# Kernel optimization log

Hardware: AMD Instinct MI355X
Metric: run time of the kernel (lower is better)

## Reference

```python
import jax, jax.numpy as jnp
import numpy as np

B, T = 64, 2048
HID, FAST, SLOW, VOCAB = 256, 64, 256, 64
WRITE_THRESH = 0.4
NEG = -1000000000.0


def setup_inputs() -> dict:
    key = jax.random.key(0)
    ks = jax.random.split(key, 10)
    s = 0.05  # small init so gate sigmoids are not saturated
    return {
        "seq": jax.random.randint(ks[0], (B, T), 0, VOCAB),
        "emb": jax.random.normal(ks[1], (VOCAB, HID), jnp.float32),        # encoder embedding table
        "Wg": jax.random.normal(ks[2], (HID, 1), jnp.float32) * s,         # write_gate
        "bg": jnp.zeros((1,), jnp.float32),
        "Wd": jax.random.normal(ks[3], (HID, 1), jnp.float32) * s,         # demotion_net
        "bd": jnp.zeros((1,), jnp.float32),
        "Wq": jax.random.normal(ks[4], (HID, HID), jnp.float32) * s,       # read_head.q_proj
        "bq": jnp.zeros((HID,), jnp.float32),
        "Wo": jax.random.normal(ks[5], (HID, VOCAB), jnp.float32) * s,     # read_head.out
        "bo": jnp.zeros((VOCAB,), jnp.float32),
    }


def _process_sequence(h, Wg, bg, Wd, bd):
    # h: (B, T, H). Sequential LRU tiered-memory scatter, vectorized over batch.
    Bb, Tt, H = h.shape

    def step(state, tok_h):
        fm, sm, fa, sa, fu, su = state
        ws = jax.nn.sigmoid(tok_h @ Wg + bg)[:, 0]          # (B,) write score
        act = ws >= WRITE_THRESH                            # skip rows with score < 0.4
        fa = fa + fu.astype(jnp.int32)                      # age occupied slots
        sa = sa + su.astype(jnp.int32)
        free = ~fu
        has_free = jnp.any(free, axis=1)                    # (B,)
        free_idx = jnp.argmax(free, axis=1)                 # first free fast slot
        dem = ((fm @ Wd)[..., 0] + bd[0])                   # (B, FAST) demotion scores
        dem_slot = jnp.argmin(dem, axis=1)
        fslot = jnp.where(has_free, free_idx, dem_slot)     # fast slot to write
        foh = jax.nn.one_hot(fslot, FAST, dtype=bool)
        wf = act[:, None] & foh                              # (B, FAST) fast-write mask
        # value demoted to slow (only used when fast was full)
        demoted = jnp.take_along_axis(fm, fslot[:, None, None], axis=1)[:, 0, :]
        slow_act = act & ~has_free
        sfree = ~su
        s_has_free = jnp.any(sfree, axis=1)
        ss = jnp.where(s_has_free, jnp.argmax(sfree, axis=1), jnp.argmax(sa, axis=1))
        soh = jax.nn.one_hot(ss, SLOW, dtype=bool)
        wsm = slow_act[:, None] & soh                        # (B, SLOW) slow-write mask
        sm = jnp.where(wsm[..., None], demoted[:, None, :], sm)
        sa = jnp.where(wsm, 0, sa)
        su = su | wsm
        tok = jax.lax.stop_gradient(tok_h)                   # original writes tok_h.detach()
        fm = jnp.where(wf[..., None], tok[:, None, :], fm)
        fa = jnp.where(wf, 0, fa)
        fu = fu | wf
        return (fm, sm, fa, sa, fu, su), None

    init = (
        jnp.zeros((Bb, FAST, H), h.dtype),
        jnp.zeros((Bb, SLOW, H), h.dtype),
        jnp.zeros((Bb, FAST), jnp.int32),
        jnp.zeros((Bb, SLOW), jnp.int32),
        jnp.zeros((Bb, FAST), bool),
        jnp.zeros((Bb, SLOW), bool),
    )
    hs = jnp.swapaxes(h[:, : Tt - 3], 0, 1)                  # loop runs for T-3 tokens
    (fm, sm, fa, sa, fu, su), _ = jax.lax.scan(step, init, hs)
    memory = jnp.concatenate([fm, sm], axis=1)               # (B, F+S, H)
    mask = jnp.concatenate([fu, su], axis=1).astype(h.dtype)
    slow_mask = su.astype(h.dtype)
    return memory, mask, slow_mask


def reference(seq, emb, Wg, bg, Wd, bd, Wq, bq, Wo, bo):
    h = emb[seq]                                             # encoder: (B, T, H)
    memory, mask, slow_mask = _process_sequence(h, Wg, bg, Wd, bd)
    # ReadHead
    q = h[:, -1, :] @ Wq + bq                                # (B, H)
    scores = jnp.einsum("bnh,bh->bn", memory, q)
    scores = jnp.where(mask == 0, NEG, scores)
    attn = jax.nn.softmax(scores, axis=-1)
    ctx = jnp.einsum("bn,bnh->bh", attn, memory)
    logits = ctx @ Wo + bo                                   # (B, VOCAB)
    return logits, slow_mask
```

## Files before the change

### kernel.cpp

```cpp
#include <hip/hip_runtime.h>
#include <math.h>

#define BB 64
#define TT 2048
#define HIDD 256
#define FASTN 64
#define SLOWN 256
#define VOC 64
#define TLOOP (TT - 3)
#define NEGC -1000000000.0f
#define EPAD 257
#define NEGBIG (-(1 << 20))
#define BYTEAT(U, J) ((int)(((U) >> (8 * (J))) & 0xFFu))

__global__ __launch_bounds__(512) void k_one(
    const int* __restrict__ seq, const float* __restrict__ emb,
    const float* __restrict__ Wg, const float* __restrict__ bg,
    const float* __restrict__ Wd, const float* __restrict__ bd,
    const float* __restrict__ Wq, const float* __restrict__ bq,
    const float* __restrict__ Wo, const float* __restrict__ bo,
    float* __restrict__ out) {
  const int b = blockIdx.x;
  const int tid = threadIdx.x;
  const int lane = tid & 63;
  const int wv = tid >> 6;

  __shared__ float embS[VOC * EPAD];
  __shared__ float WoS[HIDD * VOC];
  __shared__ __align__(16) unsigned char zsB[2080];
  __shared__ float qLastS[HIDD], ctxS[HIDD];
  __shared__ float pp[4][64];
  __shared__ float gp8[8][64], dp8[8][64];
  __shared__ float qp2[2][HIDD];
  __shared__ float demS[64], wS[64];
  __shared__ int prS[64], invS[64], cntTok[64];
  __shared__ int CS[8];
  __shared__ int PsS[8][64], QsS[8][64], aEndS[8][64], eSS[8][64];

  const int4 sq = ((const int4*)(seq + b * TT))[tid];
  const int lastv = seq[b * TT + TT - 1];
  const float4* emb4 = (const float4*)emb;
  for (int i = tid; i < VOC * 64; i += 512) {
    float4 e = emb4[i];
    float* d = &embS[(i >> 6) * EPAD + ((i & 63) << 2)];
    d[0] = e.x; d[1] = e.y; d[2] = e.z; d[3] = e.w;
  }
  {
    const float4* Wo4 = (const float4*)Wo;
    float4* WoS4 = (float4*)WoS;
    for (int i = tid; i < HIDD * VOC / 4; i += 512) WoS4[i] = Wo4[i];
  }
  __syncthreads();

  {
    const int v = tid & 63, kp = tid >> 6;
    const float* er = &embS[v * EPAD + kp * 32];
    const float* wg = &Wg[kp * 32];
    const float* wd = &Wd[kp * 32];
    float g = 0.f, d = 0.f;
#pragma unroll 8
    for (int k = 0; k < 32; ++k) { float e = er[k]; g += e * wg[k]; d += e * wd[k]; }
    gp8[kp][v] = g; dp8[kp][v] = d;
  }
  __syncthreads();
  if (tid < 64) {
    float g = bg[0], d = bd[0];
#pragma unroll
    for (int p = 0; p < 8; ++p) { g += gp8[p][tid]; d += dp8[p][tid]; }
    int act = (1.f / (1.f + expf(-g)) >= 0.4f) ? 1 : 0;
    demS[tid] = d;
    prS[tid] = act;
  }
  __syncthreads();
  if (tid < 64) {
    float dv = demS[tid];
    int r = 0;
    for (int u2 = 0; u2 < 64; ++u2) {
      float du = demS[u2];
      r += (du < dv || (du == dv && u2 < tid)) ? 1 : 0;
    }
    invS[r] = tid;
    prS[tid] = prS[tid] ? r : 0xFF;
  }
  __syncthreads();

  const int t0 = tid * 4;
  int tk[4] = {sq.x, sq.y, sq.z, sq.w};
  int by[4]; int c = 0;
#pragma unroll
  for (int j = 0; j < 4; ++j) {
    int r = prS[tk[j]];
    by[j] = (t0 + j < TLOOP) ? r : 0xFF;
    c += (by[j] != 0xFF) ? 1 : 0;
  }
  int incl = c;
  for (int s = 1; s < 64; s <<= 1) {
    int t = __shfl_up(incl, s);
    if (lane >= s) incl += t;
  }
  if (lane == 63) CS[wv] = incl;
  __syncthreads();

  int Ow = 0, A = 0;
#pragma unroll
  for (int w2 = 0; w2 < 8; ++w2) {
    int cw = CS[w2];
    Ow += (w2 < wv) ? cw : 0;
    A += cw;
  }
  {
    int pos = Ow + incl - c;
#pragma unroll
    for (int j = 0; j < 4; ++j)
      if (by[j] != 0xFF) zsB[pos++] = (unsigned char)by[j];
  }
  __syncthreads();

  const int fsplit = A < 64 ? A : 64;
  const int nL = A - fsplit;
  const int win = nL < 256 ? nL : 256;
  const int wstart = A - win;
  const int L = (((A + 7) >> 3) + 15) & ~15;
  const int baseW = wv * L;
  const int endW = min(baseW + L, A);

  int P = 0, Q = NEGBIG;
  for (int g = baseW; g < endW; g += 16) {
    uint4 t4 = *(const uint4*)(zsB + g);
    unsigned dsw[4] = {t4.x, t4.y, t4.z, t4.w};
    const int gHi = min(g + 16, endW);
    if (gHi == g + 16 && gHi <= fsplit) {
#pragma unroll
      for (int d = 0; d < 4; ++d)
#pragma unroll
        for (int j = 0; j < 4; ++j) {
          int x = (BYTEAT(dsw[d], j) <= lane) ? 1 : 0;
          P += x; Q += x;
        }
    } else if (gHi == g + 16 && g >= fsplit) {
#pragma unroll
      for (int d = 0; d < 4; ++d)
#pragma unroll
        for (int j = 0; j < 4; ++j) {
          int x = (BYTEAT(dsw[d], j) <= lane) ? 1 : 0;
          P += x - 1;
          Q = max(Q + x - 1, x);
        }
    } else {
#pragma unroll
      for (int d = 0; d < 4; ++d)
#pragma unroll
        for (int j = 0; j < 4; ++j) {
          int i = g + d * 4 + j;
          int x = (BYTEAT(dsw[d], j) <= lane) ? 1 : 0;
          bool vld = i < endW;
          bool fil = i < fsplit;
          int p = fil ? x : x - 1;
          int q = fil ? NEGBIG : x;
          int Pn = P + p;
          int Qn = max(Q + p, q);
          P = vld ? Pn : P;
          Q = vld ? Qn : Q;
        }
    }
  }
  PsS[wv][lane] = P;
  QsS[wv][lane] = Q;
  __syncthreads();

  int a = 0;
  for (int w2 = 0; w2 < wv; ++w2)
    a = max(a + PsS[w2][lane], QsS[w2][lane]);

  int e = 0;
  for (int g = baseW; g < endW; g += 16) {
    uint4 t4 = *(const uint4*)(zsB + g);
    unsigned dsw[4] = {t4.x, t4.y, t4.z, t4.w};
    const int gHi = min(g + 16, endW);
    const bool full = (gHi == g + 16);
    if (full && gHi <= fsplit) {
#pragma unroll
      for (int d = 0; d < 4; ++d)
#pragma unroll
        for (int j = 0; j < 4; ++j)
          a += (BYTEAT(dsw[d], j) <= lane) ? 1 : 0;
    } else if (full && g >= fsplit && gHi <= wstart) {
#pragma unroll
      for (int d = 0; d < 4; ++d)
#pragma unroll
        for (int j = 0; j < 4; ++j) {
          int xm1 = (BYTEAT(dsw[d], j) <= lane) ? 0 : -1;
          a = max(a, 1) + xm1;
        }
    } else if (full && g >= wstart) {
#pragma unroll
      for (int d = 0; d < 4; ++d)
#pragma unroll
        for (int j = 0; j < 4; ++j) {
          int xm1 = (BYTEAT(dsw[d], j) <= lane) ? 0 : -1;
          e += (a > 0) ? 1 : 0;
          a = max(a, 1) + xm1;
        }
    } else {
#pragma unroll
      for (int d = 0; d < 4; ++d)
#pragma unroll
        for (int j = 0; j < 4; ++j) {
          int i = g + d * 4 + j;
          int x = (BYTEAT(dsw[d], j) <= lane) ? 1 : 0;
          bool vld = i < endW;
          bool fil = i < fsplit;
          bool wg = vld && (i >= wstart);
          e += (wg && a > 0) ? 1 : 0;
          int af = a + x;
          int al = max(a, 1) + (x - 1);
          int an = fil ? af : al;
          a = vld ? an : a;
        }
    }
  }
  aEndS[wv][lane] = a;
  eSS[wv][lane] = e;
  __syncthreads();

  if (tid < 64) {
    int af = aEndS[7][lane];
    int et = 0;
#pragma unroll
    for (int w2 = 0; w2 < 8; ++w2) et += eSS[w2][lane];
    int ap = __shfl_up(af, 1); if (lane == 0) ap = 0;
    int ep = __shfl_up(et, 1); if (lane == 0) ep = 0;
    cntTok[invS[lane]] = (af - ap) + (et - ep);
  }

  {
    const int j = tid & 255, half = tid >> 8;
    const float* eL = &embS[lastv * EPAD + half * 128];
    const float* wq = &Wq[(half * 128) * HIDD + j];
    float acc = 0.f;
#pragma unroll 8
    for (int k = 0; k < 128; ++k) acc += eL[k] * wq[k * HIDD];
    qp2[half][j] = acc;
  }
  __syncthreads();
  if (tid < 256) qLastS[tid] = qp2[0][tid] + qp2[1][tid] + bq[tid];
  __syncthreads();

  if (tid < 256) {
    int v = tid & 63, part = tid >> 6;
    const float* er = &embS[v * EPAD + part * 64];
    const float* qr = &qLastS[part * 64];
    float s = 0.f;
#pragma unroll 8
    for (int k = 0; k < 64; ++k) s += er[k] * qr[k];
    pp[part][v] = s;
  }
  __syncthreads();
  if (tid < 64) {
    float sc = pp[0][tid] + pp[1][tid] + pp[2][tid] + pp[3][tid];
    int cc = cntTok[tid];
    float m = (cc > 0) ? sc : NEGC;
    for (int off = 32; off; off >>= 1) m = fmaxf(m, __shfl_xor(m, off));
    float w = (cc > 0) ? (float)cc * expf(sc - m) : 0.f;
    float z = w;
    for (int off = 32; off; off >>= 1) z += __shfl_xor(z, off);
    z += (float)(FASTN + SLOWN - (fsplit + win)) * expf(NEGC - m);
    wS[tid] = w / z;
  }
  __syncthreads();

  if (tid < 256) {
    float cacc = 0.f;
#pragma unroll 8
    for (int u = 0; u < 64; ++u) cacc += wS[u] * embS[u * EPAD + tid];
    ctxS[tid] = cacc;
  }
  __syncthreads();

  if (tid < 256) {
    int o = tid & 63, part = tid >> 6;
    const float* cr = &ctxS[part * 64];
    const float* wr = &WoS[part * 64 * VOC + o];
    float s = 0.f;
#pragma unroll 8
    for (int k = 0; k < 64; ++k) s += cr[k] * wr[k * VOC];
    pp[part][o] = s;
  }
  __syncthreads();
  if (tid < 64)
    out[b * VOC + tid] = pp[0][tid] + pp[1][tid] + pp[2][tid] + pp[3][tid] + bo[tid];
  if (tid < 256)
    out[BB * VOC + b * SLOWN + tid] = (tid < win) ? 1.0f : 0.0f;
}

extern "C" void kernel_launch(void* const* d_in, const int* in_sizes, int n_in,
                              void* d_out, int out_size, void* d_ws, size_t ws_size,
                              hipStream_t stream) {
  const int*   seq = (const int*)d_in[0];
  const float* emb = (const float*)d_in[1];
  const float* Wg  = (const float*)d_in[2];
  const float* bg  = (const float*)d_in[3];
  const float* Wd  = (const float*)d_in[4];
  const float* bd  = (const float*)d_in[5];
  const float* Wq  = (const float*)d_in[6];
  const float* bq  = (const float*)d_in[7];
  const float* Wo  = (const float*)d_in[8];
  const float* bo  = (const float*)d_in[9];
  float* out = (float*)d_out;

  k_one<<<dim3(64), dim3(512), 0, stream>>>(seq, emb, Wg, bg, Wd, bd,
                                            Wq, bq, Wo, bo, out);
}
```

Baseline: 94.71 us.

## Split block into scan and query warp groups to overlap work

The block is split so four warps handle the token compaction and LRU scan (8 tokens per thread) while the other four compute the last-token query projection, score partials and slow-mask output in parallel. The demotion-rank loop now uses wave shuffles instead of shared memory, which removes a barrier. Wo is no longer staged into LDS and is read directly from global memory in the output projection. These changes aim to cut serial phases and barriers, at the cost of the scan running on half as many warps with longer per-warp segments.

```diff
diff --git a/kernel.cpp b/kernel.cpp
--- a/kernel.cpp
+++ b/kernel.cpp
@@ -26,29 +26,25 @@
   const int wv = tid >> 6;
 
   __shared__ float embS[VOC * EPAD];
-  __shared__ float WoS[HIDD * VOC];
   __shared__ __align__(16) unsigned char zsB[2080];
   __shared__ float qLastS[HIDD], ctxS[HIDD];
   __shared__ float pp[4][64];
   __shared__ float gp8[8][64], dp8[8][64];
-  __shared__ float qp2[2][HIDD];
-  __shared__ float demS[64], wS[64];
+  __shared__ float wS[64];
   __shared__ int prS[64], invS[64], cntTok[64];
-  __shared__ int CS[8];
-  __shared__ int PsS[8][64], QsS[8][64], aEndS[8][64], eSS[8][64];
-
-  const int4 sq = ((const int4*)(seq + b * TT))[tid];
+  __shared__ int CS[4];
+  __shared__ int PsS[4][64], QsS[4][64], aEndS[4][64], eSS[4][64];
+
+  const int4* seq4 = (const int4*)(seq + b * TT);
+  int4 sqa = make_int4(0, 0, 0, 0), sqb = make_int4(0, 0, 0, 0);
+  if (tid < 256) { sqa = seq4[2 * tid]; sqb = seq4[2 * tid + 1]; }
   const int lastv = seq[b * TT + TT - 1];
+
   const float4* emb4 = (const float4*)emb;
   for (int i = tid; i < VOC * 64; i += 512) {
     float4 e = emb4[i];
     float* d = &embS[(i >> 6) * EPAD + ((i & 63) << 2)];
     d[0] = e.x; d[1] = e.y; d[2] = e.z; d[3] = e.w;
-  }
-  {
-    const float4* Wo4 = (const float4*)Wo;
-    float4* WoS4 = (float4*)WoS;
-    for (int i = tid; i < HIDD * VOC / 4; i += 512) WoS4[i] = Wo4[i];
   }
   __syncthreads();
 
@@ -63,200 +59,196 @@
     gp8[kp][v] = g; dp8[kp][v] = d;
   }
   __syncthreads();
+
+  float qacc = 0.f;
   if (tid < 64) {
-    float g = bg[0], d = bd[0];
-#pragma unroll
-    for (int p = 0; p < 8; ++p) { g += gp8[p][tid]; d += dp8[p][tid]; }
+    float g = bg[0], dv = bd[0];
+#pragma unroll
+    for (int p = 0; p < 8; ++p) { g += gp8[p][tid]; dv += dp8[p][tid]; }
     int act = (1.f / (1.f + expf(-g)) >= 0.4f) ? 1 : 0;
-    demS[tid] = d;
-    prS[tid] = act;
-  }
-  __syncthreads();
-  if (tid < 64) {
-    float dv = demS[tid];
     int r = 0;
-    for (int u2 = 0; u2 < 64; ++u2) {
-      float du = demS[u2];
-      r += (du < dv || (du == dv && u2 < tid)) ? 1 : 0;
+#pragma unroll
+    for (int s = 1; s < 64; ++s) {
+      float du = __shfl_xor(dv, s);
+      int u = lane ^ s;
+      r += (du < dv || (du == dv && u < lane)) ? 1 : 0;
     }
     invS[r] = tid;
-    prS[tid] = prS[tid] ? r : 0xFF;
-  }
-  __syncthreads();
-
-  const int t0 = tid * 4;
-  int tk[4] = {sq.x, sq.y, sq.z, sq.w};
-  int by[4]; int c = 0;
-#pragma unroll
-  for (int j = 0; j < 4; ++j) {
-    int r = prS[tk[j]];
-    by[j] = (t0 + j < TLOOP) ? r : 0xFF;
-    c += (by[j] != 0xFF) ? 1 : 0;
-  }
-  int incl = c;
-  for (int s = 1; s < 64; s <<= 1) {
-    int t = __shfl_up(incl, s);
-    if (lane >= s) incl += t;
-  }
-  if (lane == 63) CS[wv] = incl;
-  __syncthreads();
-
-  int Ow = 0, A = 0;
-#pragma unroll
-  for (int w2 = 0; w2 < 8; ++w2) {
-    int cw = CS[w2];
-    Ow += (w2 < wv) ? cw : 0;
-    A += cw;
-  }
-  {
-    int pos = Ow + incl - c;
-#pragma unroll
-    for (int j = 0; j < 4; ++j)
-      if (by[j] != 0xFF) zsB[pos++] = (unsigned char)by[j];
-  }
-  __syncthreads();
-
+    prS[tid] = act ? r : 0xFF;
+  } else if (tid >= 256) {
+    const int j = tid - 256;
+    const float* eL = &embS[lastv * EPAD];
+#pragma unroll 8
+    for (int k = 0; k < 128; ++k) qacc += eL[k] * Wq[k * HIDD + j];
+  }
+  __syncthreads();
+
+  int by[8], cAct = 0, incl = 0;
+  if (tid < 256) {
+    const int t0 = tid * 8;
+    int tk[8] = {sqa.x, sqa.y, sqa.z, sqa.w, sqb.x, sqb.y, sqb.z, sqb.w};
+#pragma unroll
+    for (int j = 0; j < 8; ++j) {
+      int r = prS[tk[j]];
+      by[j] = (t0 + j < TLOOP) ? r : 0xFF;
+      cAct += (by[j] != 0xFF) ? 1 : 0;
+    }
+    incl = cAct;
+    for (int s = 1; s < 64; s <<= 1) {
+      int t = __shfl_up(incl, s);
+      if (lane >= s) incl += t;
+    }
+    if (lane == 63) CS[wv] = incl;
+  } else {
+    const int j = tid - 256;
+    const float* eL = &embS[lastv * EPAD];
+#pragma unroll 8
+    for (int k = 128; k < 256; ++k) qacc += eL[k] * Wq[k * HIDD + j];
+    qLastS[j] = qacc + bq[j];
+  }
+  __syncthreads();
+
+  const int A = CS[0] + CS[1] + CS[2] + CS[3];
   const int fsplit = A < 64 ? A : 64;
   const int nL = A - fsplit;
   const int win = nL < 256 ? nL : 256;
   const int wstart = A - win;
-  const int L = (((A + 7) >> 3) + 15) & ~15;
-  const int baseW = wv * L;
-  const int endW = min(baseW + L, A);
-
-  int P = 0, Q = NEGBIG;
-  for (int g = baseW; g < endW; g += 16) {
-    uint4 t4 = *(const uint4*)(zsB + g);
-    unsigned dsw[4] = {t4.x, t4.y, t4.z, t4.w};
-    const int gHi = min(g + 16, endW);
-    if (gHi == g + 16 && gHi <= fsplit) {
-#pragma unroll
-      for (int d = 0; d < 4; ++d)
-#pragma unroll
-        for (int j = 0; j < 4; ++j) {
-          int x = (BYTEAT(dsw[d], j) <= lane) ? 1 : 0;
-          P += x; Q += x;
-        }
-    } else if (gHi == g + 16 && g >= fsplit) {
-#pragma unroll
-      for (int d = 0; d < 4; ++d)
-#pragma unroll
-        for (int j = 0; j < 4; ++j) {
-          int x = (BYTEAT(dsw[d], j) <= lane) ? 1 : 0;
-          P += x - 1;
-          Q = max(Q + x - 1, x);
-        }
-    } else {
-#pragma unroll
-      for (int d = 0; d < 4; ++d)
-#pragma unroll
-        for (int j = 0; j < 4; ++j) {
-          int i = g + d * 4 + j;
-          int x = (BYTEAT(dsw[d], j) <= lane) ? 1 : 0;
-          bool vld = i < endW;
-          bool fil = i < fsplit;
-          int p = fil ? x : x - 1;
-          int q = fil ? NEGBIG : x;
-          int Pn = P + p;
-          int Qn = max(Q + p, q);
-          P = vld ? Pn : P;
-          Q = vld ? Qn : Q;
-        }
-    }
-  }
-  PsS[wv][lane] = P;
-  QsS[wv][lane] = Q;
-  __syncthreads();
-
-  int a = 0;
-  for (int w2 = 0; w2 < wv; ++w2)
-    a = max(a + PsS[w2][lane], QsS[w2][lane]);
-
-  int e = 0;
-  for (int g = baseW; g < endW; g += 16) {
-    uint4 t4 = *(const uint4*)(zsB + g);
-    unsigned dsw[4] = {t4.x, t4.y, t4.z, t4.w};
-    const int gHi = min(g + 16, endW);
-    const bool full = (gHi == g + 16);
-    if (full && gHi <= fsplit) {
-#pragma unroll
-      for (int d = 0; d < 4; ++d)
-#pragma unroll
-        for (int j = 0; j < 4; ++j)
-          a += (BYTEAT(dsw[d], j) <= lane) ? 1 : 0;
-    } else if (full && g >= fsplit && gHi <= wstart) {
-#pragma unroll
-      for (int d = 0; d < 4; ++d)
-#pragma unroll
-        for (int j = 0; j < 4; ++j) {
-          int xm1 = (BYTEAT(dsw[d], j) <= lane) ? 0 : -1;
-          a = max(a, 1) + xm1;
-        }
-    } else if (full && g >= wstart) {
-#pragma unroll
-      for (int d = 0; d < 4; ++d)
-#pragma unroll
-        for (int j = 0; j < 4; ++j) {
-          int xm1 = (BYTEAT(dsw[d], j) <= lane) ? 0 : -1;
-          e += (a > 0) ? 1 : 0;
-          a = max(a, 1) + xm1;
-        }
-    } else {
-#pragma unroll
-      for (int d = 0; d < 4; ++d)
-#pragma unroll
-        for (int j = 0; j < 4; ++j) {
-          int i = g + d * 4 + j;
-          int x = (BYTEAT(dsw[d], j) <= lane) ? 1 : 0;
-          bool vld = i < endW;
-          bool fil = i < fsplit;
-          bool wg = vld && (i >= wstart);
-          e += (wg && a > 0) ? 1 : 0;
-          int af = a + x;
-          int al = max(a, 1) + (x - 1);
-          int an = fil ? af : al;
-          a = vld ? an : a;
-        }
-    }
-  }
-  aEndS[wv][lane] = a;
-  eSS[wv][lane] = e;
+  const int L = (((A + 3) >> 2) + 15) & ~15;
+
+  if (tid < 256) {
+    int Ow = 0;
+#pragma unroll
+    for (int w2 = 0; w2 < 4; ++w2) Ow += (w2 < wv) ? CS[w2] : 0;
+    int pos = Ow + incl - cAct;
+#pragma unroll
+    for (int j = 0; j < 8; ++j)
+      if (by[j] != 0xFF) zsB[pos++] = (unsigned char)by[j];
+  } else {
+    const int j = tid - 256;
+    out[BB * VOC + b * SLOWN + j] = (j < win) ? 1.0f : 0.0f;
+  }
+  __syncthreads();
+
+  if (tid < 256) {
+    const int baseW = wv * L;
+    const int endW = min(baseW + L, A);
+    int P = 0, Q = NEGBIG;
+    for (int g = baseW; g < endW; g += 16) {
+      uint4 t4 = *(const uint4*)(zsB + g);
+      unsigned dsw[4] = {t4.x, t4.y, t4.z, t4.w};
+      const int gHi = min(g + 16, endW);
+      if (gHi == g + 16 && gHi <= fsplit) {
+#pragma unroll
+        for (int d = 0; d < 4; ++d)
+#pragma unroll
+          for (int j = 0; j < 4; ++j) {
+            int x = (BYTEAT(dsw[d], j) <= lane) ? 1 : 0;
+            P += x; Q += x;
+          }
+      } else if (gHi == g + 16 && g >= fsplit) {
+#pragma unroll
+        for (int d = 0; d < 4; ++d)
+#pragma unroll
+          for (int j = 0; j < 4; ++j) {
+            int x = (BYTEAT(dsw[d], j) <= lane) ? 1 : 0;
+            P += x - 1;
+            Q = max(Q + x - 1, x);
+          }
+      } else {
+#pragma unroll
+        for (int d = 0; d < 4; ++d)
+#pragma unroll
+          for (int j = 0; j < 4; ++j) {
+            int i = g + d * 4 + j;
+            int x = (BYTEAT(dsw[d], j) <= lane) ? 1 : 0;
+            bool vld = i < endW;
+            bool fil = i < fsplit;
+            int p = fil ? x : x - 1;
+            int q = fil ? NEGBIG : x;
+            int Pn = P + p;
+            int Qn = max(Q + p, q);
+            P = vld ? Pn : P;
+            Q = vld ? Qn : Q;
+          }
+      }
+    }
+    PsS[wv][lane] = P;
+    QsS[wv][lane] = Q;
+  } else {
+    const int v = tid & 63, part = wv - 4;
+    const float* er = &embS[v * EPAD + part * 64];
+    const float* qr = &qLastS[part * 64];
+    float s = 0.f;
+#pragma unroll 8
+    for (int k = 0; k < 64; ++k) s += er[k] * qr[k];
+    pp[part][v] = s;
+  }
+  __syncthreads();
+
+  if (tid < 256) {
+    int a = 0;
+    for (int w2 = 0; w2 < wv; ++w2)
+      a = max(a + PsS[w2][lane], QsS[w2][lane]);
+    int e = 0;
+    const int baseW = wv * L;
+    const int endW = min(baseW + L, A);
+    for (int g = baseW; g < endW; g += 16) {
+      uint4 t4 = *(const uint4*)(zsB + g);
+      unsigned dsw[4] = {t4.x, t4.y, t4.z, t4.w};
+      const int gHi = min(g + 16, endW);
+      const bool full = (gHi == g + 16);
+      if (full && gHi <= fsplit) {
+#pragma unroll
+        for (int d = 0; d < 4; ++d)
+#pragma unroll
+          for (int j = 0; j < 4; ++j)
+            a += (BYTEAT(dsw[d], j) <= lane) ? 1 : 0;
+      } else if (full && g >= fsplit && gHi <= wstart) {
+#pragma unroll
+        for (int d = 0; d < 4; ++d)
+#pragma unroll
+          for (int j = 0; j < 4; ++j) {
+            int xm1 = (BYTEAT(dsw[d], j) <= lane) ? 0 : -1;
+            a = max(a, 1) + xm1;
+          }
+      } else if (full && g >= wstart) {
+#pragma unroll
+        for (int d = 0; d < 4; ++d)
+#pragma unroll
+          for (int j = 0; j < 4; ++j) {
+            int xm1 = (BYTEAT(dsw[d], j) <= lane) ? 0 : -1;
+            e += (a > 0) ? 1 : 0;
+            a = max(a, 1) + xm1;
+          }
+      } else {
+#pragma unroll
+        for (int d = 0; d < 4; ++d)
+#pragma unroll
+          for (int j = 0; j < 4; ++j) {
+            int i = g + d * 4 + j;
+            int x = (BYTEAT(dsw[d], j) <= lane) ? 1 : 0;
+            bool vld = i < endW;
+            bool fil = i < fsplit;
+            bool wg = vld && (i >= wstart);
+            e += (wg && a > 0) ? 1 : 0;
+            int af = a + x;
+            int al = max(a, 1) + (x - 1);
+            int an = fil ? af : al;
+            a = vld ? an : a;
+          }
+      }
+    }
+    aEndS[wv][lane] = a;
+    eSS[wv][lane] = e;
+  }
   __syncthreads();
 
   if (tid < 64) {
-    int af = aEndS[7][lane];
-    int et = 0;
-#pragma unroll
-    for (int w2 = 0; w2 < 8; ++w2) et += eSS[w2][lane];
+    int af = aEndS[3][lane];
+    int et = eSS[0][lane] + eSS[1][lane] + eSS[2][lane] + eSS[3][lane];
     int ap = __shfl_up(af, 1); if (lane == 0) ap = 0;
     int ep = __shfl_up(et, 1); if (lane == 0) ep = 0;
     cntTok[invS[lane]] = (af - ap) + (et - ep);
-  }
-
-  {
-    const int j = tid & 255, half = tid >> 8;
-    const float* eL = &embS[lastv * EPAD + half * 128];
-    const float* wq = &Wq[(half * 128) * HIDD + j];
-    float acc = 0.f;
-#pragma unroll 8
-    for (int k = 0; k < 128; ++k) acc += eL[k] * wq[k * HIDD];
-    qp2[half][j] = acc;
-  }
-  __syncthreads();
-  if (tid < 256) qLastS[tid] = qp2[0][tid] + qp2[1][tid] + bq[tid];
-  __syncthreads();
-
-  if (tid < 256) {
-    int v = tid & 63, part = tid >> 6;
-    const float* er = &embS[v * EPAD + part * 64];
-    const float* qr = &qLastS[part * 64];
-    float s = 0.f;
-#pragma unroll 8
-    for (int k = 0; k < 64; ++k) s += er[k] * qr[k];
-    pp[part][v] = s;
-  }
-  __syncthreads();
-  if (tid < 64) {
     float sc = pp[0][tid] + pp[1][tid] + pp[2][tid] + pp[3][tid];
     int cc = cntTok[tid];
     float m = (cc > 0) ? sc : NEGC;
@@ -278,9 +270,9 @@
   __syncthreads();
 
   if (tid < 256) {
-    int o = tid & 63, part = tid >> 6;
+    const int o = tid & 63, part = tid >> 6;
     const float* cr = &ctxS[part * 64];
-    const float* wr = &WoS[part * 64 * VOC + o];
+    const float* wr = &Wo[part * 64 * VOC + o];
     float s = 0.f;
 #pragma unroll 8
     for (int k = 0; k < 64; ++k) s += cr[k] * wr[k * VOC];
@@ -289,8 +281,6 @@
   __syncthreads();
   if (tid < 64)
     out[b * VOC + tid] = pp[0][tid] + pp[1][tid] + pp[2][tid] + pp[3][tid] + bo[tid];
-  if (tid < 256)
-    out[BB * VOC + b * SLOWN + tid] = (tid < win) ? 1.0f : 0.0f;
 }
 
 extern "C" void kernel_launch(void* const* d_in, const int* in_sizes, int n_in,
```

New measurement: 102.7 us. 8.5% more time.
